# Kernel tuning notes

Hardware: AMD Instinct MI355X
Metric: run time of the kernel (lower is better)

Reference implementation:

```python
import jax, jax.numpy as jnp
import numpy as np

NUM_USER = 100000
NUM_ENT = 200000
NUM_REL = 32
DIM = 64
N_NEIGHBOR = 16
BATCH = 16384


def setup_inputs() -> dict:
    key = jax.random.key(0)
    ks = jax.random.split(key, 11)
    inp = {
        "u": jax.random.randint(ks[0], (BATCH,), 0, NUM_USER),
        "v": jax.random.randint(ks[1], (BATCH,), 0, NUM_ENT),
        "user_neighbor": jax.random.randint(ks[2], (BATCH, N_NEIGHBOR), 0, NUM_ENT),
        "item_neighbor": jax.random.randint(ks[3], (BATCH, N_NEIGHBOR), 0, NUM_USER),
        "adj_ent": jax.random.randint(ks[4], (NUM_ENT, N_NEIGHBOR), 0, NUM_ENT),
        "adj_rel": jax.random.randint(ks[5], (NUM_ENT, N_NEIGHBOR), 0, NUM_REL),
        "usr_emb": jax.random.normal(ks[6], (NUM_USER, DIM), dtype=jnp.float32) * 0.1,
        "ent_emb": jax.random.normal(ks[7], (NUM_ENT, DIM), dtype=jnp.float32) * 0.1,
        "rel_emb": jax.random.normal(ks[8], (NUM_REL, DIM), dtype=jnp.float32) * 0.1,
        "agg_W": jax.random.normal(ks[9], (DIM, DIM), dtype=jnp.float32) * (1.0 / np.sqrt(DIM)),
        "agg_b": jax.random.normal(ks[10], (DIM,), dtype=jnp.float32) * 0.01,
    }
    return inp


def reference(u, v, user_neighbor, item_neighbor, adj_ent, adj_rel,
              usr_emb, ent_emb, rel_emb, agg_W, agg_b):
    n = N_NEIGHBOR
    # LightGCN-style "lite" embeddings: mean over sampled interaction neighbors
    lite_user = usr_emb[item_neighbor].sum(axis=1) * (1.0 / n)   # [B, D]
    lite_item = ent_emb[user_neighbor].sum(axis=1) * (1.0 / n)   # [B, D]

    user_embeddings = usr_emb[u]                                  # [B, D]
    item_embeddings_original = ent_emb[v]                         # [B, D]

    # one-hop KG neighbors of items
    nbr_ent = adj_ent[v]                                          # [B, n]
    nbr_rel = adj_rel[v]                                          # [B, n]
    self_vectors = item_embeddings_original[:, None, :]           # [B, 1, D]
    neighbor_vectors = ent_emb[nbr_ent][:, None, :, :]            # [B, 1, n, D]
    neighbor_relations = rel_emb[nbr_rel][:, None, :, :]          # [B, 1, n, D]

    # KGCN sum-aggregator: user-relation attention over neighbors
    ur_scores = jnp.einsum("bd,bknd->bkn", user_embeddings, neighbor_relations)
    attn = jax.nn.softmax(ur_scores, axis=-1)                     # [B, 1, n]
    neighbors_agg = jnp.einsum("bkn,bknd->bkd", attn, neighbor_vectors)
    combined = self_vectors + neighbors_agg                       # [B, 1, D]
    item_embeddings = jnp.tanh(combined @ agg_W + agg_b)[:, 0, :]  # [B, D]

    user_final = 0.5 * lite_user + 0.5 * user_embeddings
    item_final = 0.5 * lite_item + 0.5 * item_embeddings
    scores = jnp.sum(user_final * item_final, axis=1)
    return jax.nn.sigmoid(scores)
```

## Files before the change

### kernel.cpp

```cpp
#include <hip/hip_runtime.h>
#include <math.h>

#define DIM 64
#define NNB 16
#define BATCH 16384

typedef float4 f4;

__device__ __forceinline__ float dot4(const f4 a, const f4 b) {
    return fmaf(a.x, b.x, fmaf(a.y, b.y, fmaf(a.z, b.z, a.w * b.w)));
}

__device__ __forceinline__ f4 xgrp_sum(f4 v) {
    v.x += __shfl_xor(v.x, 16, 64); v.y += __shfl_xor(v.y, 16, 64);
    v.z += __shfl_xor(v.z, 16, 64); v.w += __shfl_xor(v.w, 16, 64);
    v.x += __shfl_xor(v.x, 32, 64); v.y += __shfl_xor(v.y, 32, 64);
    v.z += __shfl_xor(v.z, 32, 64); v.w += __shfl_xor(v.w, 32, 64);
    return v;
}

template <int WPB>
__global__ __launch_bounds__(WPB * 64, 4) void klgcn_kernel(
    const int* __restrict__ u, const int* __restrict__ v,
    const int* __restrict__ user_neighbor, const int* __restrict__ item_neighbor,
    const int* __restrict__ adj_ent, const int* __restrict__ adj_rel,
    const float* __restrict__ usr_emb, const float* __restrict__ ent_emb,
    const float* __restrict__ rel_emb, const float* __restrict__ agg_W,
    const float* __restrict__ agg_b, float* __restrict__ out)
{
    const int wave = threadIdx.x >> 6;
    const int lane = threadIdx.x & 63;
    const int g = lane >> 4;
    const int s = lane & 15;
    const int b = __builtin_amdgcn_readfirstlane(blockIdx.x * WPB + wave);

    const f4* __restrict__ usr4 = (const f4*)usr_emb;
    const f4* __restrict__ ent4 = (const f4*)ent_emb;
    const f4* __restrict__ rel4 = (const f4*)rel_emb;
    const f4* __restrict__ W4   = (const f4*)agg_W;
    const f4* __restrict__ b4p  = (const f4*)agg_b;
    const int4* __restrict__ it4 = (const int4*)item_neighbor;
    const int4* __restrict__ un4 = (const int4*)user_neighbor;
    const int4* __restrict__ ar4 = (const int4*)adj_rel;
    const int4* __restrict__ ae4 = (const int4*)adj_ent;

    const int ub = __builtin_amdgcn_readfirstlane(u[b]);
    const int vb = __builtin_amdgcn_readfirstlane(v[b]);

    const int4 iit = it4[b * 4 + g];
    const int4 iun = un4[b * 4 + g];
    const int4 iar = ar4[vb * 4 + g];
    const int4 iae = ae4[vb * 4 + g];

    const f4 ue4 = usr4[(long)ub * 16 + s];
    const f4 ie4 = ent4[(long)vb * 16 + s];

    f4 Re[4], Ag[4], Lu[4], Li[4];
    Re[0] = rel4[iar.x * 16 + s];
    Re[1] = rel4[iar.y * 16 + s];
    Re[2] = rel4[iar.z * 16 + s];
    Re[3] = rel4[iar.w * 16 + s];
    Ag[0] = ent4[(long)iae.x * 16 + s];
    Ag[1] = ent4[(long)iae.y * 16 + s];
    Ag[2] = ent4[(long)iae.z * 16 + s];
    Ag[3] = ent4[(long)iae.w * 16 + s];
    Lu[0] = usr4[(long)iit.x * 16 + s];
    Lu[1] = usr4[(long)iit.y * 16 + s];
    Lu[2] = usr4[(long)iit.z * 16 + s];
    Lu[3] = usr4[(long)iit.w * 16 + s];
    Li[0] = ent4[(long)iun.x * 16 + s];
    Li[1] = ent4[(long)iun.y * 16 + s];
    Li[2] = ent4[(long)iun.z * 16 + s];
    Li[3] = ent4[(long)iun.w * 16 + s];

    float sc[4];
#pragma unroll
    for (int k = 0; k < 4; k++) {
        float p = dot4(ue4, Re[k]);
        p += __shfl_xor(p, 1, 64); p += __shfl_xor(p, 2, 64);
        p += __shfl_xor(p, 4, 64); p += __shfl_xor(p, 8, 64);
        sc[k] = p;
    }
    float m = fmaxf(fmaxf(sc[0], sc[1]), fmaxf(sc[2], sc[3]));
    m = fmaxf(m, __shfl_xor(m, 16, 64));
    m = fmaxf(m, __shfl_xor(m, 32, 64));
    float e[4];
    float ssum = 0.f;
#pragma unroll
    for (int k = 0; k < 4; k++) { e[k] = __expf(sc[k] - m); ssum += e[k]; }
    ssum += __shfl_xor(ssum, 16, 64);
    ssum += __shfl_xor(ssum, 32, 64);
    const float inv = 1.0f / ssum;

    f4 ag = {0.f, 0.f, 0.f, 0.f};
#pragma unroll
    for (int k = 0; k < 4; k++) {
        ag.x = fmaf(e[k], Ag[k].x, ag.x);
        ag.y = fmaf(e[k], Ag[k].y, ag.y);
        ag.z = fmaf(e[k], Ag[k].z, ag.z);
        ag.w = fmaf(e[k], Ag[k].w, ag.w);
    }
    ag = xgrp_sum(ag);

    f4 comb;
    comb.x = fmaf(ag.x, inv, ie4.x);
    comb.y = fmaf(ag.y, inv, ie4.y);
    comb.z = fmaf(ag.z, inv, ie4.z);
    comb.w = fmaf(ag.w, inv, ie4.w);
    const float cc[4] = {comb.x, comb.y, comb.z, comb.w};

    f4 lu;
    lu.x = Lu[0].x + Lu[1].x + Lu[2].x + Lu[3].x;
    lu.y = Lu[0].y + Lu[1].y + Lu[2].y + Lu[3].y;
    lu.z = Lu[0].z + Lu[1].z + Lu[2].z + Lu[3].z;
    lu.w = Lu[0].w + Lu[1].w + Lu[2].w + Lu[3].w;
    lu = xgrp_sum(lu);
    f4 li;
    li.x = Li[0].x + Li[1].x + Li[2].x + Li[3].x;
    li.y = Li[0].y + Li[1].y + Li[2].y + Li[3].y;
    li.z = Li[0].z + Li[1].z + Li[2].z + Li[3].z;
    li.w = Li[0].w + Li[1].w + Li[2].w + Li[3].w;
    li = xgrp_sum(li);

    f4 acc = {0.f, 0.f, 0.f, 0.f};
#pragma unroll
    for (int j = 0; j < 16; j++) {
        const int d = 16 * g + j;
        const float cd = __shfl(cc[j & 3], 20 * g + (j >> 2), 64);
        const f4 w = W4[d * 16 + s];
        acc.x = fmaf(cd, w.x, acc.x);
        acc.y = fmaf(cd, w.y, acc.y);
        acc.z = fmaf(cd, w.z, acc.z);
        acc.w = fmaf(cd, w.w, acc.w);
    }
    acc = xgrp_sum(acc);
    const f4 bias = b4p[s];
    f4 item4;
    item4.x = tanhf(acc.x + bias.x);
    item4.y = tanhf(acc.y + bias.y);
    item4.z = tanhf(acc.z + bias.z);
    item4.w = tanhf(acc.w + bias.w);

    f4 uf, itf;
    uf.x = 0.5f * fmaf(lu.x, 1.f / NNB, ue4.x);
    uf.y = 0.5f * fmaf(lu.y, 1.f / NNB, ue4.y);
    uf.z = 0.5f * fmaf(lu.z, 1.f / NNB, ue4.z);
    uf.w = 0.5f * fmaf(lu.w, 1.f / NNB, ue4.w);
    itf.x = 0.5f * fmaf(li.x, 1.f / NNB, item4.x);
    itf.y = 0.5f * fmaf(li.y, 1.f / NNB, item4.y);
    itf.z = 0.5f * fmaf(li.z, 1.f / NNB, item4.z);
    itf.w = 0.5f * fmaf(li.w, 1.f / NNB, item4.w);

    float p = dot4(uf, itf);
    p += __shfl_xor(p, 1, 64); p += __shfl_xor(p, 2, 64);
    p += __shfl_xor(p, 4, 64); p += __shfl_xor(p, 8, 64);

    if (lane == 0) out[b] = 1.0f / (1.0f + __expf(-p));
}

extern "C" void kernel_launch(void* const* d_in, const int* in_sizes, int n_in,
                              void* d_out, int out_size, void* d_ws, size_t ws_size,
                              hipStream_t stream)
{
    const int*   u             = (const int*)d_in[0];
    const int*   v             = (const int*)d_in[1];
    const int*   user_neighbor = (const int*)d_in[2];
    const int*   item_neighbor = (const int*)d_in[3];
    const int*   adj_ent       = (const int*)d_in[4];
    const int*   adj_rel       = (const int*)d_in[5];
    const float* usr_emb       = (const float*)d_in[6];
    const float* ent_emb       = (const float*)d_in[7];
    const float* rel_emb       = (const float*)d_in[8];
    const float* agg_W         = (const float*)d_in[9];
    const float* agg_b         = (const float*)d_in[10];
    float* out = (float*)d_out;

    constexpr int WPB = 4;
    dim3 grid(BATCH / WPB), block(WPB * 64);
    klgcn_kernel<WPB><<<grid, block, 0, stream>>>(
        u, v, user_neighbor, item_neighbor, adj_ent, adj_rel,
        usr_emb, ent_emb, rel_emb, agg_W, agg_b, out);
}
```

Measured before the change: 154.8 us.

## Gather neighbor embeddings directly into LDS via global_load_lds

```diff
diff --git a/kernel.cpp b/kernel.cpp
--- a/kernel.cpp
+++ b/kernel.cpp
@@ -19,8 +19,14 @@
     return v;
 }
 
+__device__ __forceinline__ void gload16(const void* gptr, void* lptr) {
+    __builtin_amdgcn_global_load_lds(
+        (const __attribute__((address_space(1))) void*)gptr,
+        (__attribute__((address_space(3))) void*)lptr, 16, 0, 0);
+}
+
 template <int WPB>
-__global__ __launch_bounds__(WPB * 64, 4) void klgcn_kernel(
+__global__ __launch_bounds__(WPB * 64) void klgcn_kernel(
     const int* __restrict__ u, const int* __restrict__ v,
     const int* __restrict__ user_neighbor, const int* __restrict__ item_neighbor,
     const int* __restrict__ adj_ent, const int* __restrict__ adj_rel,
@@ -34,6 +40,8 @@
     const int s = lane & 15;
     const int b = __builtin_amdgcn_readfirstlane(blockIdx.x * WPB + wave);
 
+    __shared__ f4 stage[WPB][16][64];
+
     const f4* __restrict__ usr4 = (const f4*)usr_emb;
     const f4* __restrict__ ent4 = (const f4*)ent_emb;
     const f4* __restrict__ rel4 = (const f4*)rel_emb;
@@ -47,31 +55,38 @@
     const int ub = __builtin_amdgcn_readfirstlane(u[b]);
     const int vb = __builtin_amdgcn_readfirstlane(v[b]);
 
+    const int4 iar = ar4[vb * 4 + g];
+    const int4 iae = ae4[vb * 4 + g];
     const int4 iit = it4[b * 4 + g];
     const int4 iun = un4[b * 4 + g];
-    const int4 iar = ar4[vb * 4 + g];
-    const int4 iae = ae4[vb * 4 + g];
 
     const f4 ue4 = usr4[(long)ub * 16 + s];
     const f4 ie4 = ent4[(long)vb * 16 + s];
 
-    f4 Re[4], Ag[4], Lu[4], Li[4];
-    Re[0] = rel4[iar.x * 16 + s];
-    Re[1] = rel4[iar.y * 16 + s];
-    Re[2] = rel4[iar.z * 16 + s];
-    Re[3] = rel4[iar.w * 16 + s];
-    Ag[0] = ent4[(long)iae.x * 16 + s];
-    Ag[1] = ent4[(long)iae.y * 16 + s];
-    Ag[2] = ent4[(long)iae.z * 16 + s];
-    Ag[3] = ent4[(long)iae.w * 16 + s];
-    Lu[0] = usr4[(long)iit.x * 16 + s];
-    Lu[1] = usr4[(long)iit.y * 16 + s];
-    Lu[2] = usr4[(long)iit.z * 16 + s];
-    Lu[3] = usr4[(long)iit.w * 16 + s];
-    Li[0] = ent4[(long)iun.x * 16 + s];
-    Li[1] = ent4[(long)iun.y * 16 + s];
-    Li[2] = ent4[(long)iun.z * 16 + s];
-    Li[3] = ent4[(long)iun.w * 16 + s];
+    gload16(&rel4[iar.x * 16 + s],       &stage[wave][0][0]);
+    gload16(&rel4[iar.y * 16 + s],       &stage[wave][1][0]);
+    gload16(&rel4[iar.z * 16 + s],       &stage[wave][2][0]);
+    gload16(&rel4[iar.w * 16 + s],       &stage[wave][3][0]);
+    gload16(&ent4[(long)iae.x * 16 + s], &stage[wave][4][0]);
+    gload16(&ent4[(long)iae.y * 16 + s], &stage[wave][5][0]);
+    gload16(&ent4[(long)iae.z * 16 + s], &stage[wave][6][0]);
+    gload16(&ent4[(long)iae.w * 16 + s], &stage[wave][7][0]);
+    gload16(&usr4[(long)iit.x * 16 + s], &stage[wave][8][0]);
+    gload16(&usr4[(long)iit.y * 16 + s], &stage[wave][9][0]);
+    gload16(&usr4[(long)iit.z * 16 + s], &stage[wave][10][0]);
+    gload16(&usr4[(long)iit.w * 16 + s], &stage[wave][11][0]);
+    gload16(&ent4[(long)iun.x * 16 + s], &stage[wave][12][0]);
+    gload16(&ent4[(long)iun.y * 16 + s], &stage[wave][13][0]);
+    gload16(&ent4[(long)iun.z * 16 + s], &stage[wave][14][0]);
+    gload16(&ent4[(long)iun.w * 16 + s], &stage[wave][15][0]);
+
+    asm volatile("s_waitcnt vmcnt(0)" ::: "memory");
+
+    f4 Re[4], Ag[4];
+#pragma unroll
+    for (int k = 0; k < 4; k++) Re[k] = stage[wave][k][lane];
+#pragma unroll
+    for (int k = 0; k < 4; k++) Ag[k] = stage[wave][4 + k][lane];
 
     float sc[4];
 #pragma unroll
@@ -109,17 +124,19 @@
     comb.w = fmaf(ag.w, inv, ie4.w);
     const float cc[4] = {comb.x, comb.y, comb.z, comb.w};
 
-    f4 lu;
-    lu.x = Lu[0].x + Lu[1].x + Lu[2].x + Lu[3].x;
-    lu.y = Lu[0].y + Lu[1].y + Lu[2].y + Lu[3].y;
-    lu.z = Lu[0].z + Lu[1].z + Lu[2].z + Lu[3].z;
-    lu.w = Lu[0].w + Lu[1].w + Lu[2].w + Lu[3].w;
+    f4 lu = {0.f, 0.f, 0.f, 0.f};
+#pragma unroll
+    for (int k = 0; k < 4; k++) {
+        const f4 t = stage[wave][8 + k][lane];
+        lu.x += t.x; lu.y += t.y; lu.z += t.z; lu.w += t.w;
+    }
     lu = xgrp_sum(lu);
-    f4 li;
-    li.x = Li[0].x + Li[1].x + Li[2].x + Li[3].x;
-    li.y = Li[0].y + Li[1].y + Li[2].y + Li[3].y;
-    li.z = Li[0].z + Li[1].z + Li[2].z + Li[3].z;
-    li.w = Li[0].w + Li[1].w + Li[2].w + Li[3].w;
+    f4 li = {0.f, 0.f, 0.f, 0.f};
+#pragma unroll
+    for (int k = 0; k < 4; k++) {
+        const f4 t = stage[wave][12 + k][lane];
+        li.x += t.x; li.y += t.y; li.z += t.z; li.w += t.w;
+    }
     li = xgrp_sum(li);
 
     f4 acc = {0.f, 0.f, 0.f, 0.f};
@@ -175,7 +192,7 @@
     const float* agg_b         = (const float*)d_in[10];
     float* out = (float*)d_out;
 
-    constexpr int WPB = 4;
+    constexpr int WPB = 2;
     dim3 grid(BATCH / WPB), block(WPB * 64);
     klgcn_kernel<WPB><<<grid, block, 0, stream>>>(
         u, v, user_neighbor, item_neighbor, adj_ent, adj_rel,
```

Measured after the change: 164.3 us. +6.1%, slower.
